# Kernel tuning notes

Measured on AMD Instinct MI355X. Metric: run time of the kernel, lower is better.

Reference implementation:

```python
import jax, jax.numpy as jnp
import numpy as np

FH, FW = 4, 4  # patch/filter spatial size (non-overlapping tiles)

def _to_patches(X, fh, fw):
    # X: (N, H, W, C) -> (N, P, fh, fw, C), P = (H//fh)*(W//fw)
    N, H, W, C = X.shape
    nr, nc = H // fh, W // fw
    x = X.reshape(N, nr, fh, nc, fw, C).transpose(0, 1, 3, 2, 4, 5)
    return x.reshape(N, nr * nc, fh, fw, C)

def setup_inputs() -> dict:
    key = jax.random.key(0)
    k1, k2 = jax.random.split(key)
    N, H, W, FIN, FOUT = 32, 128, 128, 32, 32
    P = (H // FH) * (W // FW)
    X = jax.random.normal(k1, (N, H, W, FIN), dtype=jnp.float32)
    filters = jax.random.normal(k2, (P, FH, FW, FIN, FOUT), dtype=jnp.float32) * 0.01  # 'alexnet' init
    bias = jnp.zeros((FOUT,), dtype=jnp.float32)
    return {"X": X, "filters": filters, "bias": bias}

def reference(X, filters, bias):
    N, H, W, C = X.shape
    nr, nc = H // FH, W // FW
    patches = _to_patches(X, FH, FW)                       # (N, P, fh, fw, fin)
    # locally-connected conv: unique filter per patch location (batched GEMM over p)
    Z = jnp.einsum('npijc,pijco->npo', patches, filters)   # (N, P, fout)
    Z = Z + bias
    A = jax.nn.relu(Z)
    return A.reshape(N, nr, nc, -1)                        # (N, H/fh, W/fw, fout)
```

## Files before the change

### kernel.cpp

```cpp
#include <hip/hip_runtime.h>


typedef __attribute__((ext_vector_type(4))) float f32x4;
typedef __attribute__((ext_vector_type(4))) short s16x4;
typedef __attribute__((ext_vector_type(8))) short s16x8;

#define HWC (128 * 128 * 32)
#define WC  (128 * 32)
#define FOUT 32
#define ROW 264

__device__ __forceinline__ short f2bf(float f) {
    unsigned u = __builtin_bit_cast(unsigned, f);
    u += 0x7fffu + ((u >> 16) & 1u);
    return (short)(u >> 16);
}

__device__ __forceinline__ void barrier_lds_only() {
    asm volatile("s_waitcnt lgkmcnt(0)" ::: "memory");
    __builtin_amdgcn_s_barrier();
    asm volatile("" ::: "memory");
}

__launch_bounds__(256, 4)
__global__ void lcconv_kernel(const float* __restrict__ X,
                              const float* __restrict__ F,
                              const float* __restrict__ bias,
                              float* __restrict__ out) {
    __shared__ short Xs[32 * ROW];
    __shared__ short Fs[32 * ROW];

    const int p    = blockIdx.x;
    const int pr   = p >> 5;
    const int pc   = p & 31;
    const int tid  = threadIdx.x;
    const int lane = tid & 63;
    const int w    = tid >> 6;
    const int mi   = (w >> 1) * 16;
    const int ni   = (w & 1) * 16;

    const int xbase = pr * 4 * WC + pc * 128;
    const float* Fp = F + p * (512 * FOUT);

    auto loadX = [&](f32x4* xv, int h) {
        #pragma unroll
        for (int it = 0; it < 8; ++it) {
            int idx = it * 256 + tid;
            int n   = idx >> 6;
            int il  = (idx >> 5) & 1;
            int w4  = idx & 31;
            xv[it] = *(const f32x4*)(X + n * HWC + xbase + (2 * h + il) * WC + w4 * 4);
        }
    };
    auto loadF = [&](f32x4* fv, int h) {
        #pragma unroll
        for (int tt = 0; tt < 2; ++tt) {
            int task = tt * 256 + tid;
            int o4   = task & 7;
            int k4   = task >> 3;
            const float* fp0 = Fp + (h * 256 + k4 * 4) * FOUT + o4 * 4;
            #pragma unroll
            for (int d = 0; d < 4; ++d)
                fv[tt * 4 + d] = *(const f32x4*)(fp0 + d * FOUT);
        }
    };
    auto storeLDS = [&](const f32x4* xv, const f32x4* fv) {
        #pragma unroll
        for (int it = 0; it < 8; ++it) {
            int idx = it * 256 + tid;
            int n   = idx >> 6;
            int il  = (idx >> 5) & 1;
            int w4  = idx & 31;
            s16x4 b;
            b[0] = f2bf(xv[it][0]); b[1] = f2bf(xv[it][1]);
            b[2] = f2bf(xv[it][2]); b[3] = f2bf(xv[it][3]);
            *(s16x4*)(&Xs[n * ROW + il * 128 + w4 * 4]) = b;
        }
        #pragma unroll
        for (int tt = 0; tt < 2; ++tt) {
            int task = tt * 256 + tid;
            int o4   = task & 7;
            int k4   = task >> 3;
            #pragma unroll
            for (int e = 0; e < 4; ++e) {
                s16x4 b;
                b[0] = f2bf(fv[tt * 4 + 0][e]); b[1] = f2bf(fv[tt * 4 + 1][e]);
                b[2] = f2bf(fv[tt * 4 + 2][e]); b[3] = f2bf(fv[tt * 4 + 3][e]);
                *(s16x4*)(&Fs[(o4 * 4 + e) * ROW + k4 * 4]) = b;
            }
        }
    };

    const int arow = mi + (lane & 15);
    const int brow = ni + (lane & 15);
    const int g16  = (lane >> 4) * 8;

    f32x4 acc = {0.f, 0.f, 0.f, 0.f};
    auto mfmaHalf = [&]() {
        #pragma unroll
        for (int ks = 0; ks < 8; ++ks) {
            s16x8 a = *(const s16x8*)(&Xs[arow * ROW + ks * 32 + g16]);
            s16x8 b = *(const s16x8*)(&Fs[brow * ROW + ks * 32 + g16]);
            acc = __builtin_amdgcn_mfma_f32_16x16x32_bf16(a, b, acc, 0, 0, 0);
        }
    };

    f32x4 xa[8], fa[8], xb[8], fb[8];

    loadX(xa, 0);
    loadF(fa, 0);
    storeLDS(xa, fa);
    loadX(xb, 1);
    loadF(fb, 1);
    barrier_lds_only();

    mfmaHalf();

    __builtin_amdgcn_s_barrier();
    asm volatile("" ::: "memory");

    storeLDS(xb, fb);
    barrier_lds_only();

    mfmaHalf();

    const int o_g = ni + (lane & 15);
    const float bv = bias[o_g];
    #pragma unroll
    for (int r = 0; r < 4; ++r) {
        int n_g = mi + (lane >> 4) * 4 + r;
        float v = acc[r] + bv;
        v = v > 0.f ? v : 0.f;
        out[n_g * (1024 * FOUT) + p * FOUT + o_g] = v;
    }
}

extern "C" void kernel_launch(void* const* d_in, const int* in_sizes, int n_in,
                              void* d_out, int out_size, void* d_ws, size_t ws_size,
                              hipStream_t stream) {
    const float* X    = (const float*)d_in[0];
    const float* F    = (const float*)d_in[1];
    const float* bias = (const float*)d_in[2];
    float* out        = (float*)d_out;
    lcconv_kernel<<<dim3(1024), dim3(256), 0, stream>>>(X, F, bias, out);
}
```

Measured before the change: 148.1 us.

## Split K across two wave groups with 512 threads and XOR-swizzled LDS

```diff
diff --git a/kernel.cpp b/kernel.cpp
--- a/kernel.cpp
+++ b/kernel.cpp
@@ -7,8 +7,6 @@
 
 #define HWC (128 * 128 * 32)
 #define WC  (128 * 32)
-#define FOUT 32
-#define ROW 264
 
 __device__ __forceinline__ short f2bf(float f) {
     unsigned u = __builtin_bit_cast(unsigned, f);
@@ -16,19 +14,17 @@
     return (short)(u >> 16);
 }
 
-__device__ __forceinline__ void barrier_lds_only() {
-    asm volatile("s_waitcnt lgkmcnt(0)" ::: "memory");
-    __builtin_amdgcn_s_barrier();
-    asm volatile("" ::: "memory");
+__device__ __forceinline__ int swz(int row, int k) {
+    return row * 512 + (k ^ ((row & 7) << 3));
 }
 
-__launch_bounds__(256, 4)
+__launch_bounds__(512, 4)
 __global__ void lcconv_kernel(const float* __restrict__ X,
                               const float* __restrict__ F,
                               const float* __restrict__ bias,
                               float* __restrict__ out) {
-    __shared__ short Xs[32 * ROW];
-    __shared__ short Fs[32 * ROW];
+    __shared__ short Xs[32 * 512];
+    __shared__ short Fs[32 * 512];
 
     const int p    = blockIdx.x;
     const int pr   = p >> 5;
@@ -36,49 +32,53 @@
     const int tid  = threadIdx.x;
     const int lane = tid & 63;
     const int w    = tid >> 6;
-    const int mi   = (w >> 1) * 16;
-    const int ni   = (w & 1) * 16;
+    const int t    = w & 3;
+    const int h    = w >> 2;
+    const int mi   = (t >> 1) * 16;
+    const int ni   = (t & 1) * 16;
 
-    const int xbase = pr * 4 * WC + pc * 128;
-    const float* Fp = F + p * (512 * FOUT);
-
-    auto loadX = [&](f32x4* xv, int h) {
+    f32x4 xv[8], fv[8];
+    {
+        const int xbase = pr * 4 * WC + pc * 128;
         #pragma unroll
         for (int it = 0; it < 8; ++it) {
-            int idx = it * 256 + tid;
-            int n   = idx >> 6;
-            int il  = (idx >> 5) & 1;
-            int w4  = idx & 31;
-            xv[it] = *(const f32x4*)(X + n * HWC + xbase + (2 * h + il) * WC + w4 * 4);
+            int idx = it * 512 + tid;
+            int n   = idx >> 7;
+            int r   = idx & 127;
+            int i   = r >> 5;
+            int w4  = r & 31;
+            xv[it] = *(const f32x4*)(X + n * HWC + xbase + i * WC + w4 * 4);
         }
-    };
-    auto loadF = [&](f32x4* fv, int h) {
+        const float* Fp = F + p * (512 * 32);
         #pragma unroll
         for (int tt = 0; tt < 2; ++tt) {
-            int task = tt * 256 + tid;
+            int task = tt * 512 + tid;
             int o4   = task & 7;
             int k4   = task >> 3;
-            const float* fp0 = Fp + (h * 256 + k4 * 4) * FOUT + o4 * 4;
+            const float* fp0 = Fp + k4 * 4 * 32 + o4 * 4;
             #pragma unroll
             for (int d = 0; d < 4; ++d)
-                fv[tt * 4 + d] = *(const f32x4*)(fp0 + d * FOUT);
+                fv[tt * 4 + d] = *(const f32x4*)(fp0 + d * 32);
         }
-    };
-    auto storeLDS = [&](const f32x4* xv, const f32x4* fv) {
+    }
+    asm volatile("" ::: "memory");
+
+    {
         #pragma unroll
         for (int it = 0; it < 8; ++it) {
-            int idx = it * 256 + tid;
-            int n   = idx >> 6;
-            int il  = (idx >> 5) & 1;
-            int w4  = idx & 31;
+            int idx = it * 512 + tid;
+            int n   = idx >> 7;
+            int r   = idx & 127;
+            int i   = r >> 5;
+            int w4  = r & 31;
             s16x4 b;
             b[0] = f2bf(xv[it][0]); b[1] = f2bf(xv[it][1]);
             b[2] = f2bf(xv[it][2]); b[3] = f2bf(xv[it][3]);
-            *(s16x4*)(&Xs[n * ROW + il * 128 + w4 * 4]) = b;
+            *(s16x4*)(&Xs[swz(n, i * 128 + w4 * 4)]) = b;
         }
         #pragma unroll
         for (int tt = 0; tt < 2; ++tt) {
-            int task = tt * 256 + tid;
+            int task = tt * 512 + tid;
             int o4   = task & 7;
             int k4   = task >> 3;
             #pragma unroll
@@ -86,52 +86,44 @@
                 s16x4 b;
                 b[0] = f2bf(fv[tt * 4 + 0][e]); b[1] = f2bf(fv[tt * 4 + 1][e]);
                 b[2] = f2bf(fv[tt * 4 + 2][e]); b[3] = f2bf(fv[tt * 4 + 3][e]);
-                *(s16x4*)(&Fs[(o4 * 4 + e) * ROW + k4 * 4]) = b;
+                *(s16x4*)(&Fs[swz(o4 * 4 + e, k4 * 4)]) = b;
             }
         }
-    };
-
-    const int arow = mi + (lane & 15);
-    const int brow = ni + (lane & 15);
-    const int g16  = (lane >> 4) * 8;
+    }
+    __syncthreads();
 
     f32x4 acc = {0.f, 0.f, 0.f, 0.f};
-    auto mfmaHalf = [&]() {
+    {
+        const int arow = mi + (lane & 15);
+        const int brow = ni + (lane & 15);
+        const int g16  = (lane >> 4) * 8;
+        const int kb   = h * 256;
         #pragma unroll
         for (int ks = 0; ks < 8; ++ks) {
-            s16x8 a = *(const s16x8*)(&Xs[arow * ROW + ks * 32 + g16]);
-            s16x8 b = *(const s16x8*)(&Fs[brow * ROW + ks * 32 + g16]);
+            s16x8 a = *(const s16x8*)(&Xs[swz(arow, kb + ks * 32 + g16)]);
+            s16x8 b = *(const s16x8*)(&Fs[swz(brow, kb + ks * 32 + g16)]);
             acc = __builtin_amdgcn_mfma_f32_16x16x32_bf16(a, b, acc, 0, 0, 0);
         }
-    };
+    }
+    __syncthreads();
 
-    f32x4 xa[8], fa[8], xb[8], fb[8];
-
-    loadX(xa, 0);
-    loadF(fa, 0);
-    storeLDS(xa, fa);
-    loadX(xb, 1);
-    loadF(fb, 1);
-    barrier_lds_only();
-
-    mfmaHalf();
-
-    __builtin_amdgcn_s_barrier();
-    asm volatile("" ::: "memory");
-
-    storeLDS(xb, fb);
-    barrier_lds_only();
-
-    mfmaHalf();
-
-    const int o_g = ni + (lane & 15);
-    const float bv = bias[o_g];
-    #pragma unroll
-    for (int r = 0; r < 4; ++r) {
-        int n_g = mi + (lane >> 4) * 4 + r;
-        float v = acc[r] + bv;
-        v = v > 0.f ? v : 0.f;
-        out[n_g * (1024 * FOUT) + p * FOUT + o_g] = v;
+    float* rbuf = (float*)Xs;
+    if (h == 1) {
+        #pragma unroll
+        for (int r = 0; r < 4; ++r)
+            rbuf[(t * 4 + r) * 64 + lane] = acc[r];
+    }
+    __syncthreads();
+    if (h == 0) {
+        const int o_g = ni + (lane & 15);
+        const float bv = bias[o_g];
+        #pragma unroll
+        for (int r = 0; r < 4; ++r) {
+            int n_g = mi + (lane >> 4) * 4 + r;
+            float v = acc[r] + rbuf[(t * 4 + r) * 64 + lane] + bv;
+            v = v > 0.f ? v : 0.f;
+            out[n_g * (1024 * 32) + p * 32 + o_g] = v;
+        }
     }
 }
 
@@ -142,5 +134,5 @@
     const float* F    = (const float*)d_in[1];
     const float* bias = (const float*)d_in[2];
     float* out        = (float*)d_out;
-    lcconv_kernel<<<dim3(1024), dim3(256), 0, stream>>>(X, F, bias, out);
+    lcconv_kernel<<<dim3(1024), dim3(512), 0, stream>>>(X, F, bias, out);
 }
```

Result: no change. 147.3 us (-0.5%).
